# Performance work log

Measured on AMD Instinct MI355X. Metric: run time of the kernel, lower is better.

Reference implementation:

```python
import jax, jax.numpy as jnp
import numpy as np

EMBED = 1024
HEADS = 16
HEAD_DIM = EMBED // HEADS
SCALE = HEAD_DIM ** -0.5


def setup_inputs() -> dict:
    key = jax.random.key(0)
    ks = jax.random.split(key, 11)
    T, B = 2048, 2
    xavier = lambda k: jax.random.uniform(k, (EMBED, EMBED), jnp.float32,
                                          -np.sqrt(6.0 / (2 * EMBED)), np.sqrt(6.0 / (2 * EMBED)))
    return {
        "query": jax.random.normal(ks[0], (T, B, EMBED), jnp.float32),
        "key": jax.random.normal(ks[1], (T, B, EMBED), jnp.float32),
        "value": jax.random.normal(ks[2], (T, B, EMBED), jnp.float32),
        "Wq": xavier(ks[3]), "bq": jnp.zeros((EMBED,), jnp.float32),
        "Wk": xavier(ks[4]), "bk": jnp.zeros((EMBED,), jnp.float32),
        "Wv": xavier(ks[5]), "bv": jnp.zeros((EMBED,), jnp.float32),
        "Wo": xavier(ks[6]), "bo": jnp.zeros((EMBED,), jnp.float32),
    }


def reference(query, key, value, Wq, bq, Wk, bk, Wv, bv, Wo, bo):
    T, B, E = query.shape
    S = key.shape[0]
    # projections (nn.Linear: x @ W.T + b)
    q = (query @ Wq.T + bq) * SCALE
    k = key @ Wk.T + bk
    v = value @ Wv.T + bv
    # [len, B, E] -> [B*H, len, hd]
    def split_heads(x, L):
        return x.reshape(L, B * HEADS, HEAD_DIM).transpose(1, 0, 2)
    q = split_heads(q, T)
    k = split_heads(k, S)
    v = split_heads(v, S)
    # scores [B*H, T, S]
    scores = jnp.einsum('btd,bsd->bts', q, k)
    attn_weights = jax.nn.softmax(scores, axis=-1)
    attn = jnp.einsum('bts,bsd->btd', attn_weights, v)  # [B*H, T, hd]
    attn = attn.transpose(1, 0, 2).reshape(T, B, E)
    out = attn @ Wo.T + bo
    avg_weights = attn_weights.reshape(B, HEADS, T, S).sum(axis=1) / HEADS
    return out, avg_weights
```

## Files before the change

### kernel.cpp

```cpp
#include <hip/hip_runtime.h>
#include <math.h>

#define T_LEN 2048
#define B_SZ 2
#define EMB 1024
#define HEADS 16
#define HD 64
#define BH (B_SZ*HEADS)
#define R_ROWS (T_LEN*B_SZ)

typedef unsigned short u16;
typedef __attribute__((ext_vector_type(8))) short bf16x8;
typedef __attribute__((ext_vector_type(4))) short bf16x4;
typedef __attribute__((ext_vector_type(4))) float f32x4;

#define MFMA32(a,b,c) __builtin_amdgcn_mfma_f32_16x16x32_bf16(a,b,c,0,0,0)
#if __has_builtin(__builtin_amdgcn_mfma_f32_16x16x16_bf16)
#define MFMA16(a,b,c) __builtin_amdgcn_mfma_f32_16x16x16_bf16(a,b,c,0,0,0)
#else
#define MFMA16(a,b,c) __builtin_amdgcn_mfma_f32_16x16x16bf16_1k(a,b,c,0,0,0)
#endif

__device__ __forceinline__ u16 f2bf(float f) {
    union { float f; unsigned int u; } v; v.f = f;
    unsigned int r = v.u + 0x7fffu + ((v.u >> 16) & 1u);
    return (u16)(r >> 16);
}
__device__ __forceinline__ float bf2f(u16 h) {
    union { unsigned int u; float f; } v; v.u = ((unsigned int)h) << 16;
    return v.f;
}
__device__ __forceinline__ ushort4 hi4(float4 x) {
    ushort4 u; u.x = f2bf(x.x); u.y = f2bf(x.y); u.z = f2bf(x.z); u.w = f2bf(x.w); return u;
}
__device__ __forceinline__ ushort4 lo4(float4 x, ushort4 h) {
    ushort4 u;
    u.x = f2bf(x.x - bf2f(h.x));
    u.y = f2bf(x.y - bf2f(h.y));
    u.z = f2bf(x.z - bf2f(h.z));
    u.w = f2bf(x.w - bf2f(h.w));
    return u;
}
__device__ __forceinline__ float exp2f_fast(float x) {
#if __has_builtin(__builtin_amdgcn_exp2f)
    return __builtin_amdgcn_exp2f(x);
#else
    float r; asm("v_exp_f32 %0, %1" : "=v"(r) : "v"(x)); return r;
#endif
}
__device__ __forceinline__ float log2f_fast(float x) {
    float r; asm("v_log_f32 %0, %1" : "=v"(r) : "v"(x)); return r;
}
__device__ __forceinline__ bf16x4 pk_bf16x4(float a, float b, float c, float d) {
    union { unsigned int u[2]; bf16x4 v; } t;
    asm("v_cvt_pk_bf16_f32 %0, %1, %2" : "=v"(t.u[0]) : "v"(a), "v"(b));
    asm("v_cvt_pk_bf16_f32 %0, %1, %2" : "=v"(t.u[1]) : "v"(c), "v"(d));
    return t.v;
}
__device__ __forceinline__ void lds_cp16(u16* lds, const u16* g) {
    __builtin_amdgcn_global_load_lds(
        (const __attribute__((address_space(1))) unsigned int*)(const void*)g,
        (__attribute__((address_space(3))) unsigned int*)(void*)lds,
        16, 0, 0);
}

__global__ __launch_bounds__(256)
void conv7_kernel(const float* __restrict__ Wq, const float* __restrict__ Wk,
                  const float* __restrict__ Wv, const float* __restrict__ Wo,
                  u16* __restrict__ WqHi, u16* __restrict__ WqLo,
                  u16* __restrict__ WkHi, u16* __restrict__ WkLo,
                  u16* __restrict__ WvHi, u16* __restrict__ WvLo,
                  u16* __restrict__ WoHi, u16* __restrict__ WoLo,
                  const float* __restrict__ xq, const float* __restrict__ xk,
                  const float* __restrict__ xv,
                  u16* __restrict__ xqHi, u16* __restrict__ xkHi,
                  u16* __restrict__ xvHi)
{
    if (blockIdx.x < 2048) {
        const int g = blockIdx.x >> 9;
        const float* src = (g == 0) ? Wq : (g == 1) ? Wk : (g == 2) ? Wv : Wo;
        u16* hi = (g == 0) ? WqHi : (g == 1) ? WkHi : (g == 2) ? WvHi : WoHi;
        u16* lo = (g == 0) ? WqLo : (g == 1) ? WkLo : (g == 2) ? WvLo : WoLo;
        size_t base = ((size_t)(blockIdx.x & 511)*256 + threadIdx.x)*8;
        float4 a = *(const float4*)(src + base);
        float4 b = *(const float4*)(src + base + 4);
        ushort4 h0 = hi4(a), h1 = hi4(b);
        *(ushort4*)(hi + base)     = h0;
        *(ushort4*)(hi + base + 4) = h1;
        *(ushort4*)(lo + base)     = lo4(a, h0);
        *(ushort4*)(lo + base + 4) = lo4(b, h1);
    } else {
        const int idx = blockIdx.x - 2048;
        const int g = idx >> 11;
        const float* src = (g == 0) ? xq : (g == 1) ? xk : xv;
        u16* hi = (g == 0) ? xqHi : (g == 1) ? xkHi : xvHi;
        size_t base = ((size_t)(idx & 2047)*256 + threadIdx.x)*8;
        float4 a = *(const float4*)(src + base);
        float4 b = *(const float4*)(src + base + 4);
        *(ushort4*)(hi + base)     = hi4(a);
        *(ushort4*)(hi + base + 4) = hi4(b);
    }
}

__device__ __forceinline__
void proj_body(u16* __restrict__ sAh, u16* __restrict__ sAl,
               u16* __restrict__ sBh, u16* __restrict__ sBl,
               const u16* __restrict__ Ahi, const u16* __restrict__ Alo,
               const u16* __restrict__ Bhi, const u16* __restrict__ Blo,
               const float* __restrict__ bias,
               float* __restrict__ outF, u16* __restrict__ outHi,
               float scale, int mode, int bxi, int byi)
{
    const int tid = threadIdx.x;
    const int w = tid >> 6, ln = tid & 63, lm = ln & 15, lq = ln >> 4;
    const int wm = w & 3, wn = w >> 2;
    const int m0 = bxi * 128, n0 = byi * 64;
    const int K = 1024;
    const int ar = ln >> 2;
    const int ac = ln & 3;
    const bool hasAl = (Alo != nullptr);
    const bool hasBl = (Blo != nullptr);

    f32x4 acc[2][2];
#pragma unroll
    for (int i = 0; i < 2; ++i)
#pragma unroll
        for (int j = 0; j < 2; ++j) acc[i][j] = (f32x4){0.f,0.f,0.f,0.f};

    auto stage = [&](int p, int k0) {
        {
            int r = w*16 + ar;
            int c = ac ^ ((r >> 1) & 3);
            size_t g = (size_t)(m0 + r)*K + k0 + c*8;
            lds_cp16(sAh + p*4096 + w*512, Ahi + g);
            if (hasAl) lds_cp16(sAl + p*4096 + w*512, Alo + g);
        }
        {
            int ch = w & 3;
            int r = ch*16 + ar;
            int c = ac ^ ((r >> 1) & 3);
            size_t g = (size_t)(n0 + r)*K + k0 + c*8;
            if (w < 4) lds_cp16(sBh + p*2048 + ch*512, Bhi + g);
            else if (hasBl) lds_cp16(sBl + p*2048 + ch*512, Blo + g);
        }
    };

    stage(0, 0);
    int cur = 0;
    for (int k0 = 0; k0 < 1024; k0 += 32) {
        __syncthreads();
        if (k0 + 32 < 1024) stage(cur ^ 1, k0 + 32);

        bf16x8 afh[2], afl[2], bfh[2], bfl[2];
#pragma unroll
        for (int i = 0; i < 2; ++i) {
            int row = wm*32 + i*16 + lm;
            int off = row*32 + (lq ^ ((row >> 1) & 3))*8;
            afh[i] = *(const bf16x8*)&sAh[cur*4096 + off];
            if (hasAl) afl[i] = *(const bf16x8*)&sAl[cur*4096 + off];
        }
#pragma unroll
        for (int j = 0; j < 2; ++j) {
            int row = wn*32 + j*16 + lm;
            int off = row*32 + (lq ^ ((row >> 1) & 3))*8;
            bfh[j] = *(const bf16x8*)&sBh[cur*2048 + off];
            if (hasBl) bfl[j] = *(const bf16x8*)&sBl[cur*2048 + off];
        }
#pragma unroll
        for (int i = 0; i < 2; ++i)
#pragma unroll
            for (int j = 0; j < 2; ++j) {
                f32x4 a = acc[i][j];
                if (hasBl) a = MFMA32(afh[i], bfl[j], a);
                if (hasAl) a = MFMA32(afl[i], bfh[j], a);
                a = MFMA32(afh[i], bfh[j], a);
                acc[i][j] = a;
            }
        cur ^= 1;
    }

    if (mode == 0) {
#pragma unroll
        for (int j = 0; j < 2; ++j) {
            float bv = bias[n0 + wn*32 + j*16 + lm];
#pragma unroll
            for (int i = 0; i < 2; ++i)
#pragma unroll
                for (int r = 0; r < 4; ++r) {
                    int gm = m0 + wm*32 + i*16 + lq*4 + r;
                    outF[(size_t)gm*EMB + n0 + wn*32 + j*16 + lm] = acc[i][j][r] + bv;
                }
        }
    } else if (mode == 1) {
        const int h = n0 >> 6;
#pragma unroll
        for (int j = 0; j < 2; ++j) {
            float bv = bias[n0 + wn*32 + j*16 + lm];
            int d = wn*32 + j*16 + lm;
#pragma unroll
            for (int i = 0; i < 2; ++i)
#pragma unroll
                for (int r = 0; r < 4; ++r) {
                    int gm = m0 + wm*32 + i*16 + lq*4 + r;
                    int t = gm >> 1, bb = gm & 1;
                    float val = (acc[i][j][r] + bv) * scale;
                    size_t o = ((size_t)(bb*HEADS + h)*T_LEN + t)*HD + d;
                    outHi[o] = f2bf(val);
                }
        }
    } else {
#pragma unroll
        for (int i = 0; i < 2; ++i)
#pragma unroll
            for (int r = 0; r < 4; ++r) {
                int gm = m0 + wm*32 + i*16 + lq*4 + r;
                int h = gm >> 6, d = gm & 63;
                float bv = bias[gm];
#pragma unroll
                for (int j = 0; j < 2; ++j) {
                    int gn = n0 + wn*32 + j*16 + lm;
                    int t = gn >> 1, bb = gn & 1;
                    outHi[((size_t)(bb*HEADS + h)*HD + d)*T_LEN + t] = f2bf(acc[i][j][r] + bv);
                }
            }
    }
}

__global__ __launch_bounds__(512)
void proj_qkv(const u16* __restrict__ xqHi, const u16* __restrict__ xkHi,
              const u16* __restrict__ xvHi,
              const u16* __restrict__ WqHi, const u16* __restrict__ WqLo,
              const u16* __restrict__ WkHi, const u16* __restrict__ WkLo,
              const u16* __restrict__ WvHi, const u16* __restrict__ WvLo,
              const float* __restrict__ bq, const float* __restrict__ bk,
              const float* __restrict__ bv,
              u16* __restrict__ qHi, u16* __restrict__ kHi, u16* __restrict__ vT,
              float qscale)
{
    __shared__ __align__(16) u16 smem[20480];
    const int z = blockIdx.y;
    if (z == 0)
        proj_body(smem, smem , smem + 8192, smem + 12288,
                  xqHi, nullptr, WqHi, WqLo, bq, nullptr, qHi,
                  qscale, 1, blockIdx.x & 31, blockIdx.x >> 5);
    else if (z == 1)
        proj_body(smem, smem , smem + 8192, smem + 12288,
                  xkHi, nullptr, WkHi, WkLo, bk, nullptr, kHi,
                  1.0f, 1, blockIdx.x & 31, blockIdx.x >> 5);
    else
        proj_body(smem, smem + 8192, smem + 16384, smem + 16384 ,
                  WvHi, WvLo, xvHi, nullptr, bv, nullptr, vT,
                  1.0f, 2, blockIdx.x & 7, blockIdx.x >> 3);
}

__global__ __launch_bounds__(256)
void flash_kernel(const u16* __restrict__ qHi,
                  const u16* __restrict__ kHi, const u16* __restrict__ vT,
                  u16* __restrict__ attnHi,
                  float* __restrict__ lbuf)
{
    __shared__ __align__(16) u16 Khi[2][64*64];
    __shared__ __align__(16) u16 Vts[2][64*64];
    const int tid = threadIdx.x;
    const int w = tid >> 6, ln = tid & 63, lm = ln & 15, lq = ln >> 4;
    const int bh = blockIdx.y;
    const int t0 = blockIdx.x * 64;
    const int b = bh >> 4, hh = bh & 15;
    const int sr = ln >> 3, scc = ln & 7;

    bf16x8 qfhi[2];
    {
        size_t qo = ((size_t)bh*T_LEN + t0 + w*16 + lm)*HD;
#pragma unroll
        for (int f = 0; f < 2; ++f)
            qfhi[f] = *(const bf16x8*)(qHi + qo + f*32 + lq*8);
    }

    const bf16x4 onesf = {(short)0x3F80, (short)0x3F80, (short)0x3F80, (short)0x3F80};

    f32x4 O[4];
    f32x4 lsum = (f32x4){0.f,0.f,0.f,0.f};
#pragma unroll
    for (int dt = 0; dt < 4; ++dt) O[dt] = (f32x4){0.f,0.f,0.f,0.f};

    auto stage = [&](int p, int s0) {
#pragma unroll
        for (int i = 0; i < 2; ++i) {
            int ch = w*2 + i;
            int r = ch*8 + sr;
            int c = scc ^ (r & 7);
            lds_cp16(&Khi[p][ch*512], kHi + ((size_t)bh*T_LEN + s0 + r)*HD + c*8);
            lds_cp16(&Vts[p][ch*512], vT  + ((size_t)bh*HD + r)*T_LEN + s0 + c*8);
        }
    };

    stage(0, 0);
    int cur = 0;
    for (int s0 = 0; s0 < T_LEN; s0 += 64) {
        __syncthreads();
        if (s0 + 64 < T_LEN) stage(cur ^ 1, s0 + 64);

        const u16* __restrict__ KH = Khi[cur];
        const u16* __restrict__ VS = Vts[cur];

        f32x4 S[4];
#pragma unroll
        for (int ms = 0; ms < 4; ++ms) {
            const int kr = ms*16 + lm;
            const int sw = kr & 7;
            const u16* rowH = &KH[kr*64];
            bf16x8 ah0 = *(const bf16x8*)(rowH + ((lq    ) ^ sw)*8);
            bf16x8 ah1 = *(const bf16x8*)(rowH + ((lq + 4) ^ sw)*8);
            __builtin_amdgcn_s_setprio(1);
            f32x4 s4 = {0.f,0.f,0.f,0.f};
            s4 = MFMA32(ah0, qfhi[0], s4);
            s4 = MFMA32(ah1, qfhi[1], s4);
            __builtin_amdgcn_s_setprio(0);
            S[ms] = s4;
        }

        bf16x4 P[4];
#pragma unroll
        for (int ms = 0; ms < 4; ++ms) {
            float p0 = exp2f_fast(S[ms][0]);
            float p1 = exp2f_fast(S[ms][1]);
            float p2 = exp2f_fast(S[ms][2]);
            float p3 = exp2f_fast(S[ms][3]);
            P[ms] = pk_bf16x4(p0, p1, p2, p3);
        }

        __builtin_amdgcn_s_setprio(1);
#pragma unroll
        for (int ms = 0; ms < 4; ++ms)
            lsum = MFMA16(P[ms], onesf, lsum);
#pragma unroll
        for (int dt = 0; dt < 4; ++dt) {
            const int d = dt*16 + lm;
            const int dw = d & 7;
#pragma unroll
            for (int ms = 0; ms < 4; ++ms) {
                bf16x4 vf = *(const bf16x4*)&VS[d*64 + ((2*ms + (lq>>1)) ^ dw)*8 + (lq&1)*4];
                O[dt] = MFMA16(P[ms], vf, O[dt]);
            }
        }
        __builtin_amdgcn_s_setprio(0);
        cur ^= 1;
    }

    {
        int tbase = t0 + w*16;
        f32x4 iv;
#pragma unroll
        for (int r = 0; r < 4; ++r) iv[r] = 1.0f / lsum[r];
        if (lm == 0) {
#pragma unroll
            for (int r = 0; r < 4; ++r)
                lbuf[(size_t)bh*T_LEN + tbase + lq*4 + r] = lsum[r];
        }
#pragma unroll
        for (int dt = 0; dt < 4; ++dt)
#pragma unroll
            for (int r = 0; r < 4; ++r) {
                int t = tbase + lq*4 + r;
                size_t o = ((size_t)t*B_SZ + b)*EMB + hh*HD + dt*16 + lm;
                attnHi[o] = f2bf(O[dt][r] * iv[r]);
            }
    }
}

__device__ __forceinline__
void avg_body(u16* __restrict__ smem,
              const u16* __restrict__ qHi, const u16* __restrict__ kHi,
              const float* __restrict__ lbuf,
              float* __restrict__ avg, int sbx, int tbx, int b)
{
    u16* Khi = smem;
    const int tid = threadIdx.x;
    const int w = tid >> 6, ln = tid & 63, lm = ln & 15, lq = ln >> 4;
    const int s0 = sbx * 128;
    const int t0 = tbx * 128;
    const int sr = ln >> 3, scc = ln & 7;
    f32x4 acc[8];
#pragma unroll
    for (int ms = 0; ms < 8; ++ms) acc[ms] = (f32x4){0.f,0.f,0.f,0.f};

    auto stage = [&](int p, int h) {
        const int bhh = b*HEADS + h;
#pragma unroll
        for (int i = 0; i < 2; ++i) {
            int ch = w*2 + i;
            int r = ch*8 + sr;
            int c = scc ^ (r & 7);
            lds_cp16(Khi + p*8192 + ch*512, kHi + ((size_t)bhh*T_LEN + s0 + r)*HD + c*8);
        }
    };

    stage(0, 0);
    int cur = 0;
    const int t = t0 + w*16 + lm;
    for (int h = 0; h < HEADS; ++h) {
        const int bh = b*HEADS + h;
        bf16x8 qfh[2];
        size_t qo = ((size_t)bh*T_LEN + t)*HD;
#pragma unroll
        for (int f = 0; f < 2; ++f)
            qfh[f] = *(const bf16x8*)(qHi + qo + f*32 + lq*8);
        float mvl = log2f_fast(lbuf[(size_t)bh*T_LEN + t]) + 4.0f;
        __syncthreads();
        if (h + 1 < HEADS) stage(cur ^ 1, h + 1);

        const u16* __restrict__ KH = Khi + cur*8192;
#pragma unroll
        for (int ms = 0; ms < 8; ++ms) {
            const int kr = ms*16 + lm;
            const int sw = kr & 7;
            const u16* rowH = &KH[kr*64];
            bf16x8 ah0 = *(const bf16x8*)(rowH + ((lq    ) ^ sw)*8);
            bf16x8 ah1 = *(const bf16x8*)(rowH + ((lq + 4) ^ sw)*8);
            f32x4 s4 = {0.f,0.f,0.f,0.f};
            s4 = MFMA32(ah0, qfh[0], s4);
            s4 = MFMA32(ah1, qfh[1], s4);
            f32x4 a = acc[ms];
            a[0] += exp2f_fast(s4[0]-mvl);
            a[1] += exp2f_fast(s4[1]-mvl);
            a[2] += exp2f_fast(s4[2]-mvl);
            a[3] += exp2f_fast(s4[3]-mvl);
            acc[ms] = a;
        }
        cur ^= 1;
    }
#pragma unroll
    for (int ms = 0; ms < 8; ++ms) {
        float4 v;
        v.x = acc[ms][0]; v.y = acc[ms][1];
        v.z = acc[ms][2]; v.w = acc[ms][3];
        *(float4*)(avg + ((size_t)b*T_LEN + t)*T_LEN + s0 + ms*16 + lq*4) = v;
    }
}

__global__ __launch_bounds__(512)
void oproj_avg(const u16* __restrict__ attnHi,
               const u16* __restrict__ WoHi, const u16* __restrict__ WoLo,
               const float* __restrict__ bo, float* __restrict__ out,
               const u16* __restrict__ qHi, const u16* __restrict__ kHi,
               const float* __restrict__ lbuf,
               float* __restrict__ avg)
{
    __shared__ __align__(16) u16 smem[16384];
    if (blockIdx.x < 512) {
        proj_body(smem, smem , smem + 8192, smem + 12288,
                  attnHi, nullptr, WoHi, WoLo, bo, out, nullptr,
                  1.0f, 0, blockIdx.x & 31, blockIdx.x >> 5);
    } else {
        const int f = blockIdx.x - 512;
        avg_body(smem, qHi, kHi, lbuf, avg,
                 f & 15, (f >> 4) & 15, f >> 8);
    }
}

extern "C" void kernel_launch(void* const* d_in, const int* in_sizes, int n_in,
                              void* d_out, int out_size, void* d_ws, size_t ws_size,
                              hipStream_t stream)
{
    const float* query = (const float*)d_in[0];
    const float* key   = (const float*)d_in[1];
    const float* value = (const float*)d_in[2];
    const float* Wq = (const float*)d_in[3];
    const float* bq = (const float*)d_in[4];
    const float* Wk = (const float*)d_in[5];
    const float* bk = (const float*)d_in[6];
    const float* Wv = (const float*)d_in[7];
    const float* bv = (const float*)d_in[8];
    const float* Wo = (const float*)d_in[9];
    const float* bo = (const float*)d_in[10];

    float* out = (float*)d_out;
    float* avg = out + (size_t)R_ROWS*EMB;

    const size_t NX = (size_t)R_ROWS*EMB;
    const size_t NW = (size_t)EMB*EMB;
    u16* wsu = (u16*)d_ws;
    u16* cHi  = wsu;            u16* cLo  = cHi + NX;
    u16* WqHi = cLo + NX;       u16* WqLo = WqHi + NW;
    u16* WkHi = WqLo + NW;      u16* WkLo = WkHi + NW;
    u16* WvHi = WkLo + NW;      u16* WvLo = WvHi + NW;
    u16* WoHi = WvLo + NW;      u16* WoLo = WoHi + NW;
    u16* qHi  = WoLo + NW;      u16* xkHi = qHi + NX;
    u16* kHi  = xkHi + NX;      u16* xvHi = kHi + NX;
    u16* vT   = xvHi + NX;
    float* lb = (float*)(vT + NX);

    const float qscale = 0.125f * 1.44269504088896340736f;

    conv7_kernel<<<8192, 256, 0, stream>>>(Wq, Wk, Wv, Wo,
                                           WqHi, WqLo, WkHi, WkLo,
                                           WvHi, WvLo, WoHi, WoLo,
                                           query, key, value,
                                           cHi, xkHi, xvHi);

    proj_qkv<<<dim3(512, 3), 512, 0, stream>>>(cHi, xkHi, xvHi,
                                               WqHi, WqLo, WkHi, WkLo, WvHi, WvLo,
                                               bq, bk, bv,
                                               qHi, kHi, vT, qscale);

    flash_kernel<<<dim3(T_LEN/64, BH), 256, 0, stream>>>(qHi, kHi, vT, cHi, lb);

    oproj_avg<<<1024, 512, 0, stream>>>(cHi, WoHi, WoLo, bo, out,
                                        qHi, kHi, lb, avg);
}
```

Measured before the change: 295.8 us.

## Remap block indices so each XCD works on a contiguous tile region

Remaps blockIdx in the QKV projection, flash attention, output projection and avg-weights kernels so that blocks dispatched round-robin to the same XCD (low 3 bits of the block id) cover a contiguous 2D tile neighbourhood or the same heads. The goal is better L2 reuse of the shared A/B tiles and K/V within each XCD's private L2, which cuts HBM/Infinity Fabric traffic. It adds index arithmetic and assumes the round-robin dispatch of blocks across 8 XCDs and grid sizes divisible by 8.

```diff
diff --git a/kernel.cpp b/kernel.cpp
--- a/kernel.cpp
+++ b/kernel.cpp
@@ -239,18 +239,25 @@
 {
     __shared__ __align__(16) u16 smem[20480];
     const int z = blockIdx.y;
-    if (z == 0)
-        proj_body(smem, smem , smem + 8192, smem + 12288,
-                  xqHi, nullptr, WqHi, WqLo, bq, nullptr, qHi,
-                  qscale, 1, blockIdx.x & 31, blockIdx.x >> 5);
-    else if (z == 1)
-        proj_body(smem, smem , smem + 8192, smem + 12288,
-                  xkHi, nullptr, WkHi, WkLo, bk, nullptr, kHi,
-                  1.0f, 1, blockIdx.x & 31, blockIdx.x >> 5);
-    else
+    const int c = blockIdx.x & 7, j = blockIdx.x >> 3;
+    if (z == 2) {
+        const int bxi = j >> 3;
+        const int byi = c*8 + (j & 7);
         proj_body(smem, smem + 8192, smem + 16384, smem + 16384 ,
                   WvHi, WvLo, xvHi, nullptr, bv, nullptr, vT,
-                  1.0f, 2, blockIdx.x & 7, blockIdx.x >> 3);
+                  1.0f, 2, bxi, byi);
+    } else {
+        const int bxi = (c & 3)*8 + (j & 7);
+        const int byi = (c >> 2)*8 + (j >> 3);
+        if (z == 0)
+            proj_body(smem, smem , smem + 8192, smem + 12288,
+                      xqHi, nullptr, WqHi, WqLo, bq, nullptr, qHi,
+                      qscale, 1, bxi, byi);
+        else
+            proj_body(smem, smem , smem + 8192, smem + 12288,
+                      xkHi, nullptr, WkHi, WkLo, bk, nullptr, kHi,
+                      1.0f, 1, bxi, byi);
+    }
 }
 
 __global__ __launch_bounds__(256)
@@ -263,8 +270,10 @@
     __shared__ __align__(16) u16 Vts[2][64*64];
     const int tid = threadIdx.x;
     const int w = tid >> 6, ln = tid & 63, lm = ln & 15, lq = ln >> 4;
-    const int bh = blockIdx.y;
-    const int t0 = blockIdx.x * 64;
+    const int id = blockIdx.x + (blockIdx.y << 5);
+    const int xc = id & 7, xj = id >> 3;
+    const int bh = xc*4 + (xj >> 5);
+    const int t0 = (xj & 31) * 64;
     const int b = bh >> 4, hh = bh & 15;
     const int sr = ln >> 3, scc = ln & 7;
 
@@ -448,13 +457,19 @@
 {
     __shared__ __align__(16) u16 smem[16384];
     if (blockIdx.x < 512) {
+        const int c = blockIdx.x & 7, j = blockIdx.x >> 3;
+        const int bxi = (c & 3)*8 + (j & 7);
+        const int byi = (c >> 2)*8 + (j >> 3);
         proj_body(smem, smem , smem + 8192, smem + 12288,
                   attnHi, nullptr, WoHi, WoLo, bo, out, nullptr,
-                  1.0f, 0, blockIdx.x & 31, blockIdx.x >> 5);
+                  1.0f, 0, bxi, byi);
     } else {
         const int f = blockIdx.x - 512;
-        avg_body(smem, qHi, kHi, lbuf, avg,
-                 f & 15, (f >> 4) & 15, f >> 8);
+        const int c = f & 7, j = f >> 3;
+        const int b   = c >> 2;
+        const int sbx = (c & 1)*8 + (j & 7);
+        const int tbx = ((c >> 1) & 1)*8 + (j >> 3);
+        avg_body(smem, qHi, kHi, lbuf, avg, sbx, tbx, b);
     }
 }
 
```

Measured after the change: 293.9 us. No clear change (-0.7%).
